# Kernel optimization log

Hardware: AMD Instinct MI355X
Metric: run time of the kernel (lower is better)

Reference implementation:

```python
import jax, jax.numpy as jnp
import numpy as np

NUM_SEGMENTS = 10000
B, S, D = 4, 200000, 64

def setup_inputs() -> dict:
    key = jax.random.key(0)
    k1, k2, k3 = jax.random.split(key, 3)
    data = jax.random.normal(k1, (B, S, D), dtype=jnp.float32)
    v = jax.random.normal(k2, (B, S, D), dtype=jnp.float32)
    segment_index = jax.random.randint(k3, (S,), 0, NUM_SEGMENTS, dtype=jnp.int32)
    return {"data": data, "v": v, "segment_index": segment_index}

def reference(data, v, segment_index):
    # data participates only in the size assertion of the torch module;
    # the forward math is an unsorted segment sum of v along dim=1.
    assert data.shape == v.shape
    # out[b, s, d] = sum_{i : segment_index[i]==s} v[b, i, d]
    out = jnp.zeros((v.shape[0], NUM_SEGMENTS, v.shape[2]), dtype=v.dtype)
    out = out.at[:, segment_index, :].add(v)
    return out
```

## Files before the change

kernel.cpp:

```cpp
#include <hip/hip_runtime.h>

constexpr int NSEG = 10000;
constexpr int BB   = 4;
constexpr int SS   = 200000;
constexpr int DD   = 64;

constexpr int CAP     = 48;
constexpr int OVF_CAP = 4096;

__global__ void bucket_kernel(const int4* __restrict__ seg4,
                              int* __restrict__ cnt,
                              int* __restrict__ ovf_cnt,
                              int* __restrict__ bucket,
                              int* __restrict__ ovf) {
    int i = blockIdx.x * blockDim.x + threadIdx.x;
    if (i >= SS / 4) return;
    int4 sg = seg4[i];
    int base = i * 4;
    int ss[4] = {sg.x, sg.y, sg.z, sg.w};
    #pragma unroll
    for (int k = 0; k < 4; ++k) {
        int s = ss[k];
        int p = atomicAdd(&cnt[s], 1);
        if (p < CAP) {
            bucket[s * CAP + p] = base + k;
        } else {
            int o = atomicAdd(ovf_cnt, 1);
            if (o < OVF_CAP) ovf[o] = base + k;
        }
    }
}

__global__ void __launch_bounds__(256)
gather_kernel(const float4* __restrict__ v4,
              const int* __restrict__ cnt,
              const int* __restrict__ bucket,
              const int* __restrict__ seg,
              const int* __restrict__ ovf_cnt,
              const int* __restrict__ ovf,
              float4* __restrict__ out4) {
    const int idx  = blockIdx.x * blockDim.x + threadIdx.x;
    const int lane = threadIdx.x & 63;
    const int d4   = lane & 15;
    const int b    = lane >> 4;
    const int s    = idx >> 6;
    if (s >= NSEG) return;

    int n = cnt[s];
    if (n > CAP) n = CAP;
    const int* bk = bucket + s * CAP;
    const float4* vb = v4 + (size_t)b * SS * 16;

    float4 acc = make_float4(0.f, 0.f, 0.f, 0.f);

    int j = 0;
    for (; j + 7 < n; j += 8) {
        int4 r0 = *(const int4*)(bk + j);
        int4 r1 = *(const int4*)(bk + j + 4);
        float4 a0 = vb[(size_t)r0.x * 16 + d4];
        float4 a1 = vb[(size_t)r0.y * 16 + d4];
        float4 a2 = vb[(size_t)r0.z * 16 + d4];
        float4 a3 = vb[(size_t)r0.w * 16 + d4];
        float4 a4 = vb[(size_t)r1.x * 16 + d4];
        float4 a5 = vb[(size_t)r1.y * 16 + d4];
        float4 a6 = vb[(size_t)r1.z * 16 + d4];
        float4 a7 = vb[(size_t)r1.w * 16 + d4];
        acc.x += ((a0.x + a1.x) + (a2.x + a3.x)) + ((a4.x + a5.x) + (a6.x + a7.x));
        acc.y += ((a0.y + a1.y) + (a2.y + a3.y)) + ((a4.y + a5.y) + (a6.y + a7.y));
        acc.z += ((a0.z + a1.z) + (a2.z + a3.z)) + ((a4.z + a5.z) + (a6.z + a7.z));
        acc.w += ((a0.w + a1.w) + (a2.w + a3.w)) + ((a4.w + a5.w) + (a6.w + a7.w));
    }
    for (; j + 3 < n; j += 4) {
        int4 r0 = *(const int4*)(bk + j);
        float4 a0 = vb[(size_t)r0.x * 16 + d4];
        float4 a1 = vb[(size_t)r0.y * 16 + d4];
        float4 a2 = vb[(size_t)r0.z * 16 + d4];
        float4 a3 = vb[(size_t)r0.w * 16 + d4];
        acc.x += (a0.x + a1.x) + (a2.x + a3.x);
        acc.y += (a0.y + a1.y) + (a2.y + a3.y);
        acc.z += (a0.z + a1.z) + (a2.z + a3.z);
        acc.w += (a0.w + a1.w) + (a2.w + a3.w);
    }
    for (; j < n; ++j) {
        int r0 = bk[j];
        float4 a0 = vb[(size_t)r0 * 16 + d4];
        acc.x += a0.x; acc.y += a0.y; acc.z += a0.z; acc.w += a0.w;
    }

    int no = *ovf_cnt;
    if (no > 0) {
        if (no > OVF_CAP) no = OVF_CAP;
        for (int t = 0; t < no; ++t) {
            int r = ovf[t];
            if (seg[r] == s) {
                float4 a0 = vb[(size_t)r * 16 + d4];
                acc.x += a0.x; acc.y += a0.y; acc.z += a0.z; acc.w += a0.w;
            }
        }
    }

    out4[((size_t)b * NSEG + s) * 16 + d4] = acc;
}

__global__ void scatter_atomic_kernel(const float4* __restrict__ v4,
                                      const int* __restrict__ seg,
                                      float* __restrict__ out) {
    const int total  = BB * SS * (DD / 4);
    const int stride = gridDim.x * blockDim.x;
    for (int idx = blockIdx.x * blockDim.x + threadIdx.x; idx < total; idx += stride) {
        const int d4 = idx & 15;
        const int t  = idx >> 4;
        const int i  = t % SS;
        const int b  = t / SS;
        const int sg = seg[i];
        const float4 val = v4[idx];
        float* o = out + ((size_t)b * NSEG + sg) * DD + d4 * 4;
        atomicAdd(o + 0, val.x);
        atomicAdd(o + 1, val.y);
        atomicAdd(o + 2, val.z);
        atomicAdd(o + 3, val.w);
    }
}

extern "C" void kernel_launch(void* const* d_in, const int* in_sizes, int n_in,
                              void* d_out, int out_size, void* d_ws, size_t ws_size,
                              hipStream_t stream) {
    const float4* v4  = (const float4*)d_in[1];
    const int*    seg = (const int*)d_in[2];

    const size_t need = (size_t)(NSEG + 1 + NSEG * CAP + OVF_CAP) * sizeof(int);
    if (ws_size < need) {
        float* out = (float*)d_out;
        hipMemsetAsync(out, 0, (size_t)out_size * sizeof(float), stream);
        scatter_atomic_kernel<<<4096, 256, 0, stream>>>(v4, seg, out);
        return;
    }

    int* cnt     = (int*)d_ws;
    int* ovf_cnt = cnt + NSEG;
    int* bucket  = ovf_cnt + 1;
    int* ovf     = bucket + NSEG * CAP;

    hipMemsetAsync(cnt, 0, (size_t)(NSEG + 1) * sizeof(int), stream);

    bucket_kernel<<<(SS / 4 + 255) / 256, 256, 0, stream>>>(
        (const int4*)seg, cnt, ovf_cnt, bucket, ovf);

    const int total = NSEG * 64;
    gather_kernel<<<(total + 255) / 256, 256, 0, stream>>>(
        v4, cnt, bucket, seg, ovf_cnt, ovf, (float4*)d_out);

    (void)in_sizes; (void)n_in; (void)out_size;
}
```

Before: 59.90 us.

## Fuse memset, bucketing and gather into one cooperative kernel with grid syncs

Replaces the memset plus two kernel launches with a single cooperative kernel that zeroes the counters, buckets rows by segment, and gathers per segment, separated by grid-wide syncs. Blocks loop over work with grid-stride loops, and the grid size is capped by occupancy and 2500 blocks. This is meant to remove launch gaps and inter-kernel overhead. In exchange it adds grid.sync costs, per-call occupancy queries on the host, and possible lower parallelism in each phase. It also drops the fallback path for an undersized workspace.

```diff
diff --git a/kernel.cpp b/kernel.cpp
--- a/kernel.cpp
+++ b/kernel.cpp
@@ -1,4 +1,7 @@
 #include <hip/hip_runtime.h>
+#include <hip/hip_cooperative_groups.h>
+
+namespace cg = cooperative_groups;
 
 constexpr int NSEG = 10000;
 constexpr int BB   = 4;
@@ -7,45 +10,40 @@
 
 constexpr int CAP     = 48;
 constexpr int OVF_CAP = 4096;
+constexpr int NTHR    = 256;
 
-__global__ void bucket_kernel(const int4* __restrict__ seg4,
-                              int* __restrict__ cnt,
-                              int* __restrict__ ovf_cnt,
-                              int* __restrict__ bucket,
-                              int* __restrict__ ovf) {
-    int i = blockIdx.x * blockDim.x + threadIdx.x;
-    if (i >= SS / 4) return;
-    int4 sg = seg4[i];
-    int base = i * 4;
-    int ss[4] = {sg.x, sg.y, sg.z, sg.w};
-    #pragma unroll
-    for (int k = 0; k < 4; ++k) {
-        int s = ss[k];
-        int p = atomicAdd(&cnt[s], 1);
-        if (p < CAP) {
-            bucket[s * CAP + p] = base + k;
-        } else {
-            int o = atomicAdd(ovf_cnt, 1);
-            if (o < OVF_CAP) ovf[o] = base + k;
+__device__ __forceinline__ void bucket_body(int gtid, int gsz,
+                                            const int4* __restrict__ seg4,
+                                            int* __restrict__ cnt,
+                                            int* __restrict__ ovf_cnt,
+                                            int* __restrict__ bucket,
+                                            int* __restrict__ ovf) {
+    for (int i = gtid; i < SS / 4; i += gsz) {
+        int4 sg = seg4[i];
+        int base = i * 4;
+        int ss[4] = {sg.x, sg.y, sg.z, sg.w};
+        #pragma unroll
+        for (int k = 0; k < 4; ++k) {
+            int s = ss[k];
+            int p = atomicAdd(&cnt[s], 1);
+            if (p < CAP) {
+                bucket[s * CAP + p] = base + k;
+            } else {
+                int o = atomicAdd(ovf_cnt, 1);
+                if (o < OVF_CAP) ovf[o] = base + k;
+            }
         }
     }
 }
 
-__global__ void __launch_bounds__(256)
-gather_kernel(const float4* __restrict__ v4,
-              const int* __restrict__ cnt,
-              const int* __restrict__ bucket,
-              const int* __restrict__ seg,
-              const int* __restrict__ ovf_cnt,
-              const int* __restrict__ ovf,
-              float4* __restrict__ out4) {
-    const int idx  = blockIdx.x * blockDim.x + threadIdx.x;
-    const int lane = threadIdx.x & 63;
-    const int d4   = lane & 15;
-    const int b    = lane >> 4;
-    const int s    = idx >> 6;
-    if (s >= NSEG) return;
-
+__device__ __forceinline__ void gather_segment(int s, int d4, int b,
+                                               const float4* __restrict__ v4,
+                                               const int* __restrict__ cnt,
+                                               const int* __restrict__ bucket,
+                                               const int* __restrict__ seg,
+                                               const int* __restrict__ ovf_cnt,
+                                               const int* __restrict__ ovf,
+                                               float4* __restrict__ out4) {
     int n = cnt[s];
     if (n > CAP) n = CAP;
     const int* bk = bucket + s * CAP;
@@ -102,24 +100,59 @@
     out4[((size_t)b * NSEG + s) * 16 + d4] = acc;
 }
 
-__global__ void scatter_atomic_kernel(const float4* __restrict__ v4,
-                                      const int* __restrict__ seg,
-                                      float* __restrict__ out) {
-    const int total  = BB * SS * (DD / 4);
-    const int stride = gridDim.x * blockDim.x;
-    for (int idx = blockIdx.x * blockDim.x + threadIdx.x; idx < total; idx += stride) {
-        const int d4 = idx & 15;
-        const int t  = idx >> 4;
-        const int i  = t % SS;
-        const int b  = t / SS;
-        const int sg = seg[i];
-        const float4 val = v4[idx];
-        float* o = out + ((size_t)b * NSEG + sg) * DD + d4 * 4;
-        atomicAdd(o + 0, val.x);
-        atomicAdd(o + 1, val.y);
-        atomicAdd(o + 2, val.z);
-        atomicAdd(o + 3, val.w);
+__global__ void __launch_bounds__(NTHR)
+fused_kernel(const float4* __restrict__ v4,
+             const int*    __restrict__ seg,
+             int*          __restrict__ cnt,
+             int*          __restrict__ ovf_cnt,
+             int*          __restrict__ bucket,
+             int*          __restrict__ ovf,
+             float4*       __restrict__ out4) {
+    cg::grid_group grid = cg::this_grid();
+    const int gtid = blockIdx.x * NTHR + threadIdx.x;
+    const int gsz  = gridDim.x * NTHR;
+
+    for (int i = gtid; i <= NSEG; i += gsz) {
+        if (i < NSEG) cnt[i] = 0;
+        else          *ovf_cnt = 0;
     }
+    grid.sync();
+
+    bucket_body(gtid, gsz, (const int4*)seg, cnt, ovf_cnt, bucket, ovf);
+    grid.sync();
+
+    const int lane = threadIdx.x & 63;
+    const int d4   = lane & 15;
+    const int b    = lane >> 4;
+    const int wid  = gtid >> 6;
+    const int nw   = gsz >> 6;
+    for (int s = wid; s < NSEG; s += nw)
+        gather_segment(s, d4, b, v4, cnt, bucket, seg, ovf_cnt, ovf, out4);
+}
+
+__global__ void bucket_kernel(const int4* __restrict__ seg4,
+                              int* __restrict__ cnt,
+                              int* __restrict__ ovf_cnt,
+                              int* __restrict__ bucket,
+                              int* __restrict__ ovf) {
+    int i = blockIdx.x * blockDim.x + threadIdx.x;
+    if (i >= SS / 4) return;
+    bucket_body(i, SS / 4 + (1 << 30), seg4, cnt, ovf_cnt, bucket, ovf);
+}
+
+__global__ void __launch_bounds__(NTHR)
+gather_kernel(const float4* __restrict__ v4,
+              const int* __restrict__ cnt,
+              const int* __restrict__ bucket,
+              const int* __restrict__ seg,
+              const int* __restrict__ ovf_cnt,
+              const int* __restrict__ ovf,
+              float4* __restrict__ out4) {
+    const int idx  = blockIdx.x * blockDim.x + threadIdx.x;
+    const int lane = threadIdx.x & 63;
+    const int s    = idx >> 6;
+    if (s >= NSEG) return;
+    gather_segment(s, lane & 15, lane >> 4, v4, cnt, bucket, seg, ovf_cnt, ovf, out4);
 }
 
 extern "C" void kernel_launch(void* const* d_in, const int* in_sizes, int n_in,
@@ -128,27 +161,30 @@
     const float4* v4  = (const float4*)d_in[1];
     const int*    seg = (const int*)d_in[2];
 
-    const size_t need = (size_t)(NSEG + 1 + NSEG * CAP + OVF_CAP) * sizeof(int);
-    if (ws_size < need) {
-        float* out = (float*)d_out;
-        hipMemsetAsync(out, 0, (size_t)out_size * sizeof(float), stream);
-        scatter_atomic_kernel<<<4096, 256, 0, stream>>>(v4, seg, out);
-        return;
-    }
-
     int* cnt     = (int*)d_ws;
     int* ovf_cnt = cnt + NSEG;
     int* bucket  = ovf_cnt + 1;
     int* ovf     = bucket + NSEG * CAP;
+    float4* out4 = (float4*)d_out;
+
+    int maxb = 0;
+    hipError_t e = hipOccupancyMaxActiveBlocksPerMultiprocessor(
+        &maxb, (const void*)fused_kernel, NTHR, 0);
+    if (e == hipSuccess && maxb > 0) {
+        int nblk = maxb * 256;
+        if (nblk > 2500) nblk = 2500;
+        void* args[] = {(void*)&v4, (void*)&seg, (void*)&cnt, (void*)&ovf_cnt,
+                        (void*)&bucket, (void*)&ovf, (void*)&out4};
+        e = hipLaunchCooperativeKernel((void*)fused_kernel,
+                                       dim3(nblk), dim3(NTHR), args, 0, stream);
+        if (e == hipSuccess) return;
+    }
 
     hipMemsetAsync(cnt, 0, (size_t)(NSEG + 1) * sizeof(int), stream);
+    bucket_kernel<<<(SS / 4 + NTHR - 1) / NTHR, NTHR, 0, stream>>>(
+        (const int4*)seg, cnt, ovf_cnt, bucket, ovf);
+    gather_kernel<<<(NSEG * 64 + NTHR - 1) / NTHR, NTHR, 0, stream>>>(
+        v4, cnt, bucket, seg, ovf_cnt, ovf, out4);
 
-    bucket_kernel<<<(SS / 4 + 255) / 256, 256, 0, stream>>>(
-        (const int4*)seg, cnt, ovf_cnt, bucket, ovf);
-
-    const int total = NSEG * 64;
-    gather_kernel<<<(total + 255) / 256, 256, 0, stream>>>(
-        v4, cnt, bucket, seg, ovf_cnt, ovf, (float4*)d_out);
-
-    (void)in_sizes; (void)n_in; (void)out_size;
+    (void)in_sizes; (void)n_in; (void)out_size; (void)ws_size;
 }
```

Measured after the change: 183.1 us. 3.06x slower.
